# Optimization experiments

Measured on AMD Instinct MI355X. Metric: run time of the kernel, lower is better.

## Reference

```python
import jax, jax.numpy as jnp
import numpy as np

B, S, G, E, NI = 128, 40000, 4000, 16, 4
H1, H2 = 1024, 256
EPS = 1e-5


def _ln(x, w, b):
    m = x.mean(-1, keepdims=True)
    v = ((x - m) ** 2).mean(-1, keepdims=True)
    return (x - m) / jnp.sqrt(v + EPS) * w + b


def setup_inputs() -> dict:
    key = jax.random.key(0)
    ks = jax.random.split(key, 20)
    x = jax.random.normal(ks[0], (B, S), dtype=jnp.float32)
    impact_indices = jax.random.randint(ks[1], (S,), 0, NI)
    # fixed SNP->gene mask: each SNP connects to exactly one gene
    gene_of_snp = jax.random.randint(ks[2], (S,), 0, G)
    mask = jnp.zeros((G, S), jnp.float32).at[gene_of_snp, jnp.arange(S)].set(1.0)
    # impact attention params
    emb = 0.02 * jax.random.normal(ks[3], (NI, E))
    proj_w = jax.random.normal(ks[4], (E, E)) * np.sqrt(2.0 / (E + E))
    proj_b = jnp.zeros((E,))
    ln_i_w, ln_i_b = jnp.ones((E,)), jnp.zeros((E,))
    scale_w = 0.005 * jax.random.normal(ks[5], (1, E)); scale_b = jnp.zeros((1,))
    bias_w = 0.005 * jax.random.normal(ks[6], (1, E)); bias_b = jnp.zeros((1,))
    # masked linear: per-row std = sqrt(1/fan_in) (gelu path)
    fan_in = jnp.clip(mask.sum(1), 1.0, None)  # [G]
    mw = jax.random.normal(ks[7], (G, S)) * jnp.sqrt(1.0 / fan_in)[:, None]
    mb = jnp.zeros((G,))
    ln1_w, ln1_b = jnp.ones((G,)), jnp.zeros((G,))
    fc1_w = jax.random.normal(ks[8], (H1, G)) * np.sqrt(2.0 / G); fc1_b = jnp.zeros((H1,))
    lnA_w, lnA_b = jnp.ones((H1,)), jnp.zeros((H1,))
    fc2_w = jax.random.normal(ks[9], (H2, H1)) * np.sqrt(2.0 / H1); fc2_b = jnp.zeros((H2,))
    lnB_w, lnB_b = jnp.ones((H2,)), jnp.zeros((H2,))
    out_w = jax.random.normal(ks[10], (1, H2)) * np.sqrt(2.0 / (H2 + 1)); out_b = jnp.zeros((1,))
    return dict(x=x, impact_indices=impact_indices, mask=mask, emb=emb,
                proj_w=proj_w, proj_b=proj_b, ln_i_w=ln_i_w, ln_i_b=ln_i_b,
                scale_w=scale_w, scale_b=scale_b, bias_w=bias_w, bias_b=bias_b,
                mw=mw, mb=mb, ln1_w=ln1_w, ln1_b=ln1_b,
                fc1_w=fc1_w, fc1_b=fc1_b, lnA_w=lnA_w, lnA_b=lnA_b,
                fc2_w=fc2_w, fc2_b=fc2_b, lnB_w=lnB_w, lnB_b=lnB_b,
                out_w=out_w, out_b=out_b)


def reference(x, impact_indices, mask, emb, proj_w, proj_b, ln_i_w, ln_i_b,
              scale_w, scale_b, bias_w, bias_b, mw, mb, ln1_w, ln1_b,
              fc1_w, fc1_b, lnA_w, lnA_b, fc2_w, fc2_b, lnB_w, lnB_b,
              out_w, out_b):
    gelu = lambda t: jax.nn.gelu(t, approximate=False)
    # SNP impact attention
    h = emb[impact_indices]                       # [S,E]
    h = h @ proj_w.T + proj_b
    h = gelu(_ln(h, ln_i_w, ln_i_b))
    scale = (h @ scale_w.T + scale_b)[:, 0]       # [S]
    bias = (h @ bias_w.T + bias_b)[:, 0]          # [S]
    attn = 2.0 * jax.nn.sigmoid(x * scale + bias) # [B,S]
    xs = x * attn
    # masked linear SNP -> gene
    g = xs @ (mw * mask).T + mb                   # [B,G]
    g = gelu(_ln(g, ln1_w, ln1_b))
    # dense MLP head
    y = gelu(_ln(g @ fc1_w.T + fc1_b, lnA_w, lnA_b))
    y = gelu(_ln(y @ fc2_w.T + fc2_b, lnB_w, lnB_b))
    return y @ out_w.T + out_b                    # [B,1]
```

## Files before the change

kernel.cpp:

```cpp
#include <hip/hip_runtime.h>
#include <hip/hip_bf16.h>

#define S_  40000
#define G_  4000
#define B_  128
#define NI_ 4
#define E_  16
#define H1_ 1024
#define H2_ 256
#define EPSF 1e-5f
#define KSPLIT 50
#define MAXH 128
#define ATT_B 128
#define DET_B 2048
#define NTILE 625
#define NCHUNK 78125

typedef unsigned uvec4 __attribute__((ext_vector_type(4)));

#define OFF_STATS ((size_t)64)
#define OFF_XST   ((size_t)1024)
#define OFF_GT    (OFF_XST + (size_t)S_ * B_)
#define OFF_Y1P   (OFF_GT  + (size_t)G_ * B_)
#define OFF_CNT   (OFF_Y1P + (size_t)KSPLIT * B_ * H1_)
#define OFF_HITS  (OFF_CNT + (size_t)4096)

__device__ __forceinline__ float gelu_f(float x) {
    return 0.5f * x * (1.0f + erff(x * 0.70710678118654752f));
}

__global__ __launch_bounds__(256) void kFused(
        const float* __restrict__ x, const int* __restrict__ ii,
        const float* __restrict__ emb, const float* __restrict__ proj_w,
        const float* __restrict__ proj_b, const float* __restrict__ ln_i_w,
        const float* __restrict__ ln_i_b, const float* __restrict__ scale_w,
        const float* __restrict__ scale_b, const float* __restrict__ bias_w,
        const float* __restrict__ bias_b, const float* __restrict__ mask,
        float* __restrict__ xs_t, int* __restrict__ cnt, int* __restrict__ hits,
        float* __restrict__ stats) {
    const int bid = blockIdx.x, tid = threadIdx.x;
    const int lane = tid & 63, wv = tid >> 6;

    if (bid >= ATT_B) {
        const int gw = (bid - ATT_B) * 4 + wv;
        const uvec4* __restrict__ m4 = (const uvec4*)mask;
        for (int c = gw; c < NCHUNK; c += DET_B * 4) {
            const int base = c * 512;
            uvec4 v[8];
#pragma unroll
            for (int u = 0; u < 8; ++u)
                v[u] = __builtin_nontemporal_load(&m4[base + u * 64 + lane]);
            unsigned or8 = 0, or4[8];
#pragma unroll
            for (int u = 0; u < 8; ++u) {
                or4[u] = v[u].x | v[u].y | v[u].z | v[u].w;
                or8 |= or4[u];
            }
            if (__any(or8 != 0)) {
#pragma unroll
                for (int u = 0; u < 8; ++u) {
                    if (or4[u]) {
                        const int f0 = (base + u * 64 + lane) * 4;
                        if (v[u].x) { int row = (f0 + 0) / S_; int sl = atomicAdd(&cnt[row], 1); if (sl < MAXH) hits[row * MAXH + sl] = (f0 + 0) - row * S_; }
                        if (v[u].y) { int row = (f0 + 1) / S_; int sl = atomicAdd(&cnt[row], 1); if (sl < MAXH) hits[row * MAXH + sl] = (f0 + 1) - row * S_; }
                        if (v[u].z) { int row = (f0 + 2) / S_; int sl = atomicAdd(&cnt[row], 1); if (sl < MAXH) hits[row * MAXH + sl] = (f0 + 2) - row * S_; }
                        if (v[u].w) { int row = (f0 + 3) / S_; int sl = atomicAdd(&cnt[row], 1); if (sl < MAXH) hits[row * MAXH + sl] = (f0 + 3) - row * S_; }
                    }
                }
            }
        }
        return;
    }

    __shared__ float tile[64][129];
    __shared__ float hs[NI_][E_];
    __shared__ float tab[8];
    if (bid == 0 && tid < 256) stats[tid] = 0.f;
    if (tid < 64) {
        const int iv = tid >> 4, e = tid & 15;
        float s = proj_b[e];
        for (int f = 0; f < E_; ++f) s += emb[iv * E_ + f] * proj_w[e * E_ + f];
        hs[iv][e] = s;
    }
    __syncthreads();
    if (tid < NI_) {
        float m = 0.f;
        for (int e = 0; e < E_; ++e) m += hs[tid][e];
        m *= (1.f / E_);
        float v = 0.f;
        for (int e = 0; e < E_; ++e) { float d = hs[tid][e] - m; v += d * d; }
        v *= (1.f / E_);
        const float r = 1.f / sqrtf(v + EPSF);
        float sc = scale_b[0], bi = bias_b[0];
        for (int e = 0; e < E_; ++e) {
            float t = (hs[tid][e] - m) * r * ln_i_w[e] + ln_i_b[e];
            t = gelu_f(t);
            sc += t * scale_w[e];
            bi += t * bias_w[e];
        }
        tab[tid] = sc;
        tab[4 + tid] = bi;
    }
    __syncthreads();
    for (int t = bid; t < NTILE; t += ATT_B) {
        const int s0 = t * 64;
        const int s  = s0 + lane;
        const int iv = ii[s];
        const float sc = tab[iv];
        const float bi = tab[4 + iv];
#pragma unroll
        for (int j = 0; j < 32; ++j) {
            int b = wv + j * 4;
            float xv = x[(size_t)b * S_ + s];
            float at = 2.f / (1.f + expf(-(xv * sc + bi)));
            tile[lane][b] = xv * at;
        }
        __syncthreads();
        const int b2 = tid & 127;
        const int lg = tid >> 7;
#pragma unroll
        for (int j = 0; j < 32; ++j) {
            int l = lg + j * 2;
            xs_t[(size_t)(s0 + l) * B_ + b2] = tile[l][b2];
        }
        __syncthreads();
    }
}

__global__ __launch_bounds__(256) void kB(const int* __restrict__ cnt,
                                          const int* __restrict__ hits,
                                          const float* __restrict__ mw,
                                          const float* __restrict__ mb,
                                          const float* __restrict__ xs_t,
                                          float* __restrict__ g_t,
                                          float* __restrict__ stats) {
    __shared__ float rowacc[8][128];
    const int lane = threadIdx.x & 63;
    const int wv   = threadIdx.x >> 6;
    const int rowbase = blockIdx.x * 8 + wv * 2;
#pragma unroll
    for (int rr = 0; rr < 2; ++rr) {
        const int row = rowbase + rr;
        const int n = min(cnt[row], MAXH);
        float a0 = 0.f, a1 = 0.f;
        for (int j = 0; j < n; ++j) {
            const int s = hits[row * MAXH + j];
            const float w = mw[(size_t)row * S_ + s];
            a0 += w * xs_t[(size_t)s * B_ + lane];
            a1 += w * xs_t[(size_t)s * B_ + 64 + lane];
        }
        const float bias = mb[row];
        a0 += bias; a1 += bias;
        g_t[(size_t)row * B_ + lane]      = a0;
        g_t[(size_t)row * B_ + 64 + lane] = a1;
        rowacc[wv * 2 + rr][lane]      = a0;
        rowacc[wv * 2 + rr][64 + lane] = a1;
    }
    __syncthreads();
    const int b = threadIdx.x & 127, half = threadIdx.x >> 7;
    float acc = 0.f;
#pragma unroll
    for (int r = 0; r < 8; ++r) {
        float v = rowacc[r][b];
        acc += half ? v * v : v;
    }
    atomicAdd(&stats[half * 128 + b], acc);
}

__global__ __launch_bounds__(256) void k6_fc1(const float* __restrict__ g_t,
                                              const float* __restrict__ stats,
                                              const float* __restrict__ ln1_w,
                                              const float* __restrict__ ln1_b,
                                              const float* __restrict__ fc1_w,
                                              float* __restrict__ y1p) {
    __shared__ float As[16 * 128];
    __shared__ float Ws[16][64];
    __shared__ float Sm[128];
    __shared__ float Sr[128];
    const int tid  = threadIdx.x;
    const int lane = tid & 63;
    const int wv   = tid >> 6;
    const int h0   = blockIdx.x * 64;
    const int kb   = blockIdx.y;
    const int k0   = kb * 80;
    const int hh   = wv * 16;
    if (tid < 128) {
        float sm = stats[tid] * (1.f / G_);
        float var = stats[128 + tid] * (1.f / G_) - sm * sm;
        Sm[tid] = sm;
        Sr[tid] = 1.f / sqrtf(var + EPSF);
    }
    float acc0[16], acc1[16];
#pragma unroll
    for (int j = 0; j < 16; ++j) { acc0[j] = 0.f; acc1[j] = 0.f; }
    __syncthreads();
    for (int ch = 0; ch < 5; ++ch) {
        const int kc = k0 + ch * 16;
        __syncthreads();
        {
#pragma unroll
            for (int half = 0; half < 2; ++half) {
                const int idx = tid * 4 + half * 1024;
                const int kk = idx >> 7, b0 = idx & 127;
                float4 g4 = *(const float4*)(g_t + (size_t)(kc + kk) * B_ + b0);
                float4 m4 = *(const float4*)(&Sm[b0]);
                float4 r4 = *(const float4*)(&Sr[b0]);
                const float w = ln1_w[kc + kk], bb = ln1_b[kc + kk];
                float4 o;
                o.x = gelu_f((g4.x - m4.x) * r4.x * w + bb);
                o.y = gelu_f((g4.y - m4.y) * r4.y * w + bb);
                o.z = gelu_f((g4.z - m4.z) * r4.z * w + bb);
                o.w = gelu_f((g4.w - m4.w) * r4.w * w + bb);
                *(float4*)(&As[idx]) = o;
            }
        }
        {
            const int h = tid & 63, q = tid >> 6;
            float4 w4 = *(const float4*)(fc1_w + (size_t)(h0 + h) * G_ + kc + q * 4);
            Ws[q * 4 + 0][h] = w4.x; Ws[q * 4 + 1][h] = w4.y;
            Ws[q * 4 + 2][h] = w4.z; Ws[q * 4 + 3][h] = w4.w;
        }
        __syncthreads();
#pragma unroll
        for (int k = 0; k < 16; ++k) {
            const float a0  = As[k * 128 + lane];
            const float a1v = As[k * 128 + 64 + lane];
            const float4* wrow = (const float4*)(&Ws[k][hh]);
#pragma unroll
            for (int jq = 0; jq < 4; ++jq) {
                float4 w4 = wrow[jq];
                acc0[jq * 4 + 0] += a0 * w4.x;  acc1[jq * 4 + 0] += a1v * w4.x;
                acc0[jq * 4 + 1] += a0 * w4.y;  acc1[jq * 4 + 1] += a1v * w4.y;
                acc0[jq * 4 + 2] += a0 * w4.z;  acc1[jq * 4 + 2] += a1v * w4.z;
                acc0[jq * 4 + 3] += a0 * w4.w;  acc1[jq * 4 + 3] += a1v * w4.w;
            }
        }
    }
    float* out0 = y1p + ((size_t)kb * B_ + lane) * H1_ + h0 + hh;
    float* out1 = out0 + (size_t)64 * H1_;
    float4* o0 = (float4*)out0;
    float4* o1 = (float4*)out1;
#pragma unroll
    for (int q = 0; q < 4; ++q) {
        o0[q] = make_float4(acc0[q*4+0], acc0[q*4+1], acc0[q*4+2], acc0[q*4+3]);
        o1[q] = make_float4(acc1[q*4+0], acc1[q*4+1], acc1[q*4+2], acc1[q*4+3]);
    }
}

__global__ __launch_bounds__(256) void k78_head(const float* __restrict__ y1p,
                                                const float* __restrict__ fc1_b,
                                                const float* __restrict__ lnA_w,
                                                const float* __restrict__ lnA_b,
                                                const float* __restrict__ fc2_w,
                                                const float* __restrict__ fc2_b,
                                                const float* __restrict__ lnB_w,
                                                const float* __restrict__ lnB_b,
                                                const float* __restrict__ out_w,
                                                const float* __restrict__ out_b,
                                                float* __restrict__ out) {
    const int b = blockIdx.x, tid = threadIdx.x, lane = tid & 63, wv = tid >> 6;
    __shared__ float a_s[H1_];
    __shared__ float y_s[H2_];
    __shared__ float red[8];
    float v[4];
    float s_ = 0.f, q_ = 0.f;
#pragma unroll
    for (int j = 0; j < 4; ++j) {
        int h = tid + j * 256;
        float s = fc1_b[h];
#pragma unroll 10
        for (int ks = 0; ks < KSPLIT; ++ks)
            s += y1p[((size_t)ks * B_ + b) * H1_ + h];
        v[j] = s; s_ += s; q_ += s * s;
    }
    for (int off = 32; off; off >>= 1) { s_ += __shfl_down(s_, off); q_ += __shfl_down(q_, off); }
    if (lane == 0) { red[wv] = s_; red[4 + wv] = q_; }
    __syncthreads();
    {
        float Ssum = red[0] + red[1] + red[2] + red[3];
        float Qsum = red[4] + red[5] + red[6] + red[7];
        float m = Ssum / 1024.f, var = Qsum / 1024.f - m * m;
        float r = 1.f / sqrtf(var + EPSF);
#pragma unroll
        for (int j = 0; j < 4; ++j) {
            int h = tid + j * 256;
            a_s[h] = gelu_f((v[j] - m) * r * lnA_w[h] + lnA_b[h]);
        }
    }
    __syncthreads();
    for (int oi = 0; oi < 64; ++oi) {
        int o = wv * 64 + oi;
        const float4* wr = (const float4*)(fc2_w + (size_t)o * H1_);
        float d = 0.f;
#pragma unroll
        for (int q = 0; q < 4; ++q) {
            float4 ww = wr[lane + 64 * q];
            float4 aa = ((const float4*)a_s)[lane + 64 * q];
            d += aa.x * ww.x + aa.y * ww.y + aa.z * ww.z + aa.w * ww.w;
        }
        for (int off = 32; off; off >>= 1) d += __shfl_down(d, off);
        if (lane == 0) y_s[o] = d + fc2_b[o];
    }
    __syncthreads();
    float yv = y_s[tid];
    float s2 = yv, q2 = yv * yv;
    for (int off = 32; off; off >>= 1) { s2 += __shfl_down(s2, off); q2 += __shfl_down(q2, off); }
    __syncthreads();
    if (lane == 0) { red[wv] = s2; red[4 + wv] = q2; }
    __syncthreads();
    float Ssum = red[0] + red[1] + red[2] + red[3];
    float Qsum = red[4] + red[5] + red[6] + red[7];
    float m = Ssum / (float)H2_, var = Qsum / (float)H2_ - m * m;
    float r = 1.f / sqrtf(var + EPSF);
    float val = gelu_f((yv - m) * r * lnB_w[tid] + lnB_b[tid]) * out_w[tid];
    __syncthreads();
    float t_ = val;
    for (int off = 32; off; off >>= 1) t_ += __shfl_down(t_, off);
    if (lane == 0) red[wv] = t_;
    __syncthreads();
    if (tid == 0)
        out[b] = red[0] + red[1] + red[2] + red[3] + out_b[0];
}

extern "C" void kernel_launch(void* const* d_in, const int* in_sizes, int n_in,
                              void* d_out, int out_size, void* d_ws, size_t ws_size,
                              hipStream_t stream) {
    const float* x       = (const float*)d_in[0];
    const int*   ii      = (const int*)  d_in[1];
    const float* mask    = (const float*)d_in[2];
    const float* emb     = (const float*)d_in[3];
    const float* proj_w  = (const float*)d_in[4];
    const float* proj_b  = (const float*)d_in[5];
    const float* ln_i_w  = (const float*)d_in[6];
    const float* ln_i_b  = (const float*)d_in[7];
    const float* scale_w = (const float*)d_in[8];
    const float* scale_b = (const float*)d_in[9];
    const float* bias_w  = (const float*)d_in[10];
    const float* bias_b  = (const float*)d_in[11];
    const float* mw      = (const float*)d_in[12];
    const float* mb      = (const float*)d_in[13];
    const float* ln1_w   = (const float*)d_in[14];
    const float* ln1_b   = (const float*)d_in[15];
    const float* fc1_w   = (const float*)d_in[16];
    const float* fc1_b   = (const float*)d_in[17];
    const float* lnA_w   = (const float*)d_in[18];
    const float* lnA_b   = (const float*)d_in[19];
    const float* fc2_w   = (const float*)d_in[20];
    const float* fc2_b   = (const float*)d_in[21];
    const float* lnB_w   = (const float*)d_in[22];
    const float* lnB_b   = (const float*)d_in[23];
    const float* out_w   = (const float*)d_in[24];
    const float* out_b   = (const float*)d_in[25];

    float* ws    = (float*)d_ws;
    float* stats = ws + OFF_STATS;
    float* xs_t  = ws + OFF_XST;
    float* g_t   = ws + OFF_GT;
    float* y1p   = ws + OFF_Y1P;
    int*   cnt   = (int*)(ws + OFF_CNT);
    int*   hits  = (int*)(ws + OFF_HITS);
    float* out   = (float*)d_out;

    hipMemsetAsync(cnt, 0, G_ * sizeof(int), stream);
    hipLaunchKernelGGL(kFused, dim3(ATT_B + DET_B), dim3(256), 0, stream,
                       x, ii, emb, proj_w, proj_b, ln_i_w, ln_i_b, scale_w, scale_b,
                       bias_w, bias_b, mask, xs_t, cnt, hits, stats);
    hipLaunchKernelGGL(kB, dim3(G_ / 8), dim3(256), 0, stream,
                       cnt, hits, mw, mb, xs_t, g_t, stats);
    hipLaunchKernelGGL(k6_fc1, dim3(16, KSPLIT), dim3(256), 0, stream,
                       g_t, stats, ln1_w, ln1_b, fc1_w, y1p);
    hipLaunchKernelGGL(k78_head, dim3(B_), dim3(256), 0, stream,
                       y1p, fc1_b, lnA_w, lnA_b, fc2_w, fc2_b, lnB_w, lnB_b, out_w, out_b, out);
}
```

Baseline: 271.8 us.

## Split fused attention/mask-detect kernel; double-buffer mask scan loads

```diff
diff --git a/kernel.cpp b/kernel.cpp
--- a/kernel.cpp
+++ b/kernel.cpp
@@ -11,71 +11,36 @@
 #define EPSF 1e-5f
 #define KSPLIT 50
 #define MAXH 128
-#define ATT_B 128
 #define DET_B 2048
+#define NW (DET_B * 4)
+#define NBATCH 156250
 #define NTILE 625
-#define NCHUNK 78125
 
 typedef unsigned uvec4 __attribute__((ext_vector_type(4)));
 
-#define OFF_STATS ((size_t)64)
-#define OFF_XST   ((size_t)1024)
+#define OFF_CNT   ((size_t)0)
+#define OFF_STATS ((size_t)4096)
+#define OFF_XST   ((size_t)8192)
 #define OFF_GT    (OFF_XST + (size_t)S_ * B_)
 #define OFF_Y1P   (OFF_GT  + (size_t)G_ * B_)
-#define OFF_CNT   (OFF_Y1P + (size_t)KSPLIT * B_ * H1_)
-#define OFF_HITS  (OFF_CNT + (size_t)4096)
+#define OFF_HITS  (OFF_Y1P + (size_t)KSPLIT * B_ * H1_)
 
 __device__ __forceinline__ float gelu_f(float x) {
     return 0.5f * x * (1.0f + erff(x * 0.70710678118654752f));
 }
 
-__global__ __launch_bounds__(256) void kFused(
+__global__ __launch_bounds__(256) void kAttn(
         const float* __restrict__ x, const int* __restrict__ ii,
         const float* __restrict__ emb, const float* __restrict__ proj_w,
         const float* __restrict__ proj_b, const float* __restrict__ ln_i_w,
         const float* __restrict__ ln_i_b, const float* __restrict__ scale_w,
         const float* __restrict__ scale_b, const float* __restrict__ bias_w,
-        const float* __restrict__ bias_b, const float* __restrict__ mask,
-        float* __restrict__ xs_t, int* __restrict__ cnt, int* __restrict__ hits,
-        float* __restrict__ stats) {
-    const int bid = blockIdx.x, tid = threadIdx.x;
+        const float* __restrict__ bias_b, float* __restrict__ xs_t) {
+    const int tid = threadIdx.x;
     const int lane = tid & 63, wv = tid >> 6;
-
-    if (bid >= ATT_B) {
-        const int gw = (bid - ATT_B) * 4 + wv;
-        const uvec4* __restrict__ m4 = (const uvec4*)mask;
-        for (int c = gw; c < NCHUNK; c += DET_B * 4) {
-            const int base = c * 512;
-            uvec4 v[8];
-#pragma unroll
-            for (int u = 0; u < 8; ++u)
-                v[u] = __builtin_nontemporal_load(&m4[base + u * 64 + lane]);
-            unsigned or8 = 0, or4[8];
-#pragma unroll
-            for (int u = 0; u < 8; ++u) {
-                or4[u] = v[u].x | v[u].y | v[u].z | v[u].w;
-                or8 |= or4[u];
-            }
-            if (__any(or8 != 0)) {
-#pragma unroll
-                for (int u = 0; u < 8; ++u) {
-                    if (or4[u]) {
-                        const int f0 = (base + u * 64 + lane) * 4;
-                        if (v[u].x) { int row = (f0 + 0) / S_; int sl = atomicAdd(&cnt[row], 1); if (sl < MAXH) hits[row * MAXH + sl] = (f0 + 0) - row * S_; }
-                        if (v[u].y) { int row = (f0 + 1) / S_; int sl = atomicAdd(&cnt[row], 1); if (sl < MAXH) hits[row * MAXH + sl] = (f0 + 1) - row * S_; }
-                        if (v[u].z) { int row = (f0 + 2) / S_; int sl = atomicAdd(&cnt[row], 1); if (sl < MAXH) hits[row * MAXH + sl] = (f0 + 2) - row * S_; }
-                        if (v[u].w) { int row = (f0 + 3) / S_; int sl = atomicAdd(&cnt[row], 1); if (sl < MAXH) hits[row * MAXH + sl] = (f0 + 3) - row * S_; }
-                    }
-                }
-            }
-        }
-        return;
-    }
-
     __shared__ float tile[64][129];
     __shared__ float hs[NI_][E_];
     __shared__ float tab[8];
-    if (bid == 0 && tid < 256) stats[tid] = 0.f;
     if (tid < 64) {
         const int iv = tid >> 4, e = tid & 15;
         float s = proj_b[e];
@@ -102,28 +67,62 @@
         tab[4 + tid] = bi;
     }
     __syncthreads();
-    for (int t = bid; t < NTILE; t += ATT_B) {
-        const int s0 = t * 64;
-        const int s  = s0 + lane;
-        const int iv = ii[s];
-        const float sc = tab[iv];
-        const float bi = tab[4 + iv];
-#pragma unroll
-        for (int j = 0; j < 32; ++j) {
-            int b = wv + j * 4;
-            float xv = x[(size_t)b * S_ + s];
-            float at = 2.f / (1.f + expf(-(xv * sc + bi)));
-            tile[lane][b] = xv * at;
-        }
-        __syncthreads();
-        const int b2 = tid & 127;
-        const int lg = tid >> 7;
-#pragma unroll
-        for (int j = 0; j < 32; ++j) {
-            int l = lg + j * 2;
-            xs_t[(size_t)(s0 + l) * B_ + b2] = tile[l][b2];
-        }
-        __syncthreads();
+    const int s0 = blockIdx.x * 64;
+    const int s  = s0 + lane;
+    const int iv = ii[s];
+    const float sc = tab[iv];
+    const float bi = tab[4 + iv];
+#pragma unroll
+    for (int j = 0; j < 32; ++j) {
+        int b = wv + j * 4;
+        float xv = x[(size_t)b * S_ + s];
+        float at = 2.f / (1.f + expf(-(xv * sc + bi)));
+        tile[lane][b] = xv * at;
+    }
+    __syncthreads();
+    const int b2 = tid & 127;
+    const int lg = tid >> 7;
+#pragma unroll
+    for (int j = 0; j < 32; ++j) {
+        int l = lg + j * 2;
+        xs_t[(size_t)(s0 + l) * B_ + b2] = tile[l][b2];
+    }
+}
+
+#define ADDHIT(f) { int row_ = (f) / S_; int sl_ = atomicAdd(&cnt[row_], 1); \
+                    if (sl_ < MAXH) hits[row_ * MAXH + sl_] = (f) - row_ * S_; }
+#define DEC1(V, q) if (V.x | V.y | V.z | V.w) { const int f0_ = (q) * 4; \
+                    if (V.x) ADDHIT(f0_ + 0); if (V.y) ADDHIT(f0_ + 1); \
+                    if (V.z) ADDHIT(f0_ + 2); if (V.w) ADDHIT(f0_ + 3); }
+#define PROCB(V0, V1, V2, V3, cc) { \
+    unsigned o_ = (V0.x|V0.y|V0.z|V0.w) | (V1.x|V1.y|V1.z|V1.w) | \
+                  (V2.x|V2.y|V2.z|V2.w) | (V3.x|V3.y|V3.z|V3.w); \
+    if (__any(o_ != 0)) { \
+        const int qb_ = (cc) * 256 + lane; \
+        DEC1(V0, qb_); DEC1(V1, qb_ + 64); DEC1(V2, qb_ + 128); DEC1(V3, qb_ + 192); \
+    } }
+#define LOADB(D0, D1, D2, D3, cc) { const int b_ = (cc) * 256 + lane; \
+    D0 = m4[b_]; D1 = m4[b_ + 64]; D2 = m4[b_ + 128]; D3 = m4[b_ + 192]; }
+
+__global__ __launch_bounds__(256) void kDetect(const float* __restrict__ mask,
+                                               int* __restrict__ cnt,
+                                               int* __restrict__ hits) {
+    const int lane = threadIdx.x & 63;
+    const int gw   = blockIdx.x * 4 + (threadIdx.x >> 6);
+    const uvec4* __restrict__ m4 = (const uvec4*)mask;
+    uvec4 A0, A1, A2, A3, B0, B1, B2, B3;
+    int ca = gw;
+    int cb = gw + NW;
+    LOADB(A0, A1, A2, A3, ca);
+    { int cbl = (cb < NBATCH) ? cb : gw; LOADB(B0, B1, B2, B3, cbl); }
+    while (ca < NBATCH) {
+        PROCB(A0, A1, A2, A3, ca);
+        const int cn = cb + NW;
+        { int cl = (cn < NBATCH) ? cn : gw; LOADB(A0, A1, A2, A3, cl); }
+        if (cb < NBATCH) PROCB(B0, B1, B2, B3, cb);
+        const int cm = cn + NW;
+        { int cl = (cm < NBATCH) ? cm : gw; LOADB(B0, B1, B2, B3, cl); }
+        ca = cn; cb = cm;
     }
 }
 
@@ -353,18 +352,19 @@
     const float* out_b   = (const float*)d_in[25];
 
     float* ws    = (float*)d_ws;
+    int*   cnt   = (int*)(ws + OFF_CNT);
     float* stats = ws + OFF_STATS;
     float* xs_t  = ws + OFF_XST;
     float* g_t   = ws + OFF_GT;
     float* y1p   = ws + OFF_Y1P;
-    int*   cnt   = (int*)(ws + OFF_CNT);
     int*   hits  = (int*)(ws + OFF_HITS);
     float* out   = (float*)d_out;
 
-    hipMemsetAsync(cnt, 0, G_ * sizeof(int), stream);
-    hipLaunchKernelGGL(kFused, dim3(ATT_B + DET_B), dim3(256), 0, stream,
+    hipMemsetAsync(cnt, 0, (4096 + 256) * sizeof(int), stream);
+    hipLaunchKernelGGL(kDetect, dim3(DET_B), dim3(256), 0, stream, mask, cnt, hits);
+    hipLaunchKernelGGL(kAttn, dim3(NTILE), dim3(256), 0, stream,
                        x, ii, emb, proj_w, proj_b, ln_i_w, ln_i_b, scale_w, scale_b,
-                       bias_w, bias_b, mask, xs_t, cnt, hits, stats);
+                       bias_w, bias_b, xs_t);
     hipLaunchKernelGGL(kB, dim3(G_ / 8), dim3(256), 0, stream,
                        cnt, hits, mw, mb, xs_t, g_t, stats);
     hipLaunchKernelGGL(k6_fc1, dim3(16, KSPLIT), dim3(256), 0, stream,
```

New measurement: 285.2 us. +4.9%, slower.
